# Kernel optimization log

Measured on AMD Instinct MI355X. Metric: run time of the kernel, lower is better.

## Reference

```python
import jax, jax.numpy as jnp
import numpy as np

B, S, E, H, P, F = 8, 512, 512, 8, 64, 2048
D = E // H  # head_dim = 64
EPS = 1e-5


def layernorm(x, g, b):
    mu = jnp.mean(x, axis=-1, keepdims=True)
    var = jnp.mean((x - mu) ** 2, axis=-1, keepdims=True)
    return (x - mu) * jax.lax.rsqrt(var + EPS) * g + b


def setup_inputs() -> dict:
    key = jax.random.key(0)
    ks = jax.random.split(key, 20)
    s = 1.0 / np.sqrt(E)
    inp = {
        "x": jax.random.normal(ks[0], (B, S, E), jnp.float32),
        "dist": jax.random.uniform(ks[1], (B, S, S), jnp.float32),
        "delatimes": jax.random.randint(ks[2], (B, S), 0, 128, jnp.int32),
        "mask": jnp.ones((B, S), jnp.int32),
        "wq_w": jax.random.uniform(ks[3], (E, E), jnp.float32, -s, s),
        "wq_b": jnp.zeros((E,), jnp.float32),
        "wk_w": jax.random.uniform(ks[4], (E, E), jnp.float32, -s, s),
        "wk_b": jnp.zeros((E,), jnp.float32),
        "wv_w": jax.random.uniform(ks[5], (E, E), jnp.float32, -s, s),
        "wv_b": jnp.zeros((E,), jnp.float32),
        "wo_w": jax.random.uniform(ks[6], (E, E), jnp.float32, -s, s),
        "wo_b": jnp.zeros((E,), jnp.float32),
        "pos_emb": jax.random.normal(ks[7], (2 * P + 1, D), jnp.float32),
        "w1": jax.random.uniform(ks[8], (E, F), jnp.float32, -s, s),
        "b1": jnp.zeros((F,), jnp.float32),
        "w2": jax.random.uniform(ks[9], (F, E), jnp.float32, -1.0 / np.sqrt(F), 1.0 / np.sqrt(F)),
        "b2": jnp.zeros((E,), jnp.float32),
        "ln1_g": jnp.ones((E,), jnp.float32),
        "ln1_b": jnp.zeros((E,), jnp.float32),
        "ln2_g": jnp.ones((E,), jnp.float32),
        "ln2_b": jnp.zeros((E,), jnp.float32),
    }
    return inp


def reference(x, dist, delatimes, mask, wq_w, wq_b, wk_w, wk_b, wv_w, wv_b,
              wo_w, wo_b, pos_emb, w1, b1, w2, b2, ln1_g, ln1_b, ln2_g, ln2_b):
    # relative-time embedding indices [B,S,S]
    rel = delatimes[:, None, :] - delatimes[:, :, None]
    idx = jnp.clip(rel, -P, P) + P
    z = pos_emb[idx]  # [B,S,S,D]

    def heads(t, w, b):
        return (t @ w + b).reshape(B, S, H, D).transpose(0, 2, 1, 3)  # [B,H,S,D]

    q = heads(x, wq_w, wq_b)
    k = heads(x, wk_w, wk_b)
    v = heads(x, wv_w, wv_b)

    scale = D ** -0.5
    scores = jnp.einsum('bhid,bhjd->bhij', q, k) + jnp.einsum('bhid,bijd->bhij', q, z)
    w = scores * scale + 0.6 * dist[:, None, :, :]
    pad = mask[:, None, None, :]  # [B,1,1,S]
    w = jnp.where(pad == 0, -1e9, w)
    aw = jax.nn.softmax(w, axis=-1)

    attn = jnp.einsum('bhij,bhjd->bhid', aw, v) + jnp.einsum('bhij,bijd->bhid', aw, z)
    concat = attn.transpose(0, 2, 1, 3).reshape(B, S, E)
    attn_out = layernorm(x + (concat @ wo_w + wo_b), ln1_g, ln1_b)

    ffn = jax.nn.relu(attn_out @ w1 + b1) @ w2 + b2
    return layernorm(attn_out + ffn, ln2_g, ln2_b)
```

## Files before the change

### kernel.cpp

```cpp
#include <hip/hip_runtime.h>
#include <hip/hip_bf16.h>

typedef __bf16 bf16x8 __attribute__((ext_vector_type(8)));
typedef float f32x4 __attribute__((ext_vector_type(4)));

#define TOKENS 4096
#define EDIM 512
#define FDIM 2048
#define SEQ 512
#define NHEAD 8
#define HDIM 64
#define QKVS 1536

__global__ __launch_bounds__(256) void prep(
    const float* __restrict__ wq_w, const float* __restrict__ wk_w,
    const float* __restrict__ wv_w, const float* __restrict__ wo_w,
    const float* __restrict__ w1, const float* __restrict__ w2,
    const float* __restrict__ x, const float* __restrict__ dist,
    const float* __restrict__ wq_b, const float* __restrict__ wk_b,
    const float* __restrict__ wv_b,
    __bf16* __restrict__ wqkvt, __bf16* __restrict__ wot,
    __bf16* __restrict__ w1t, __bf16* __restrict__ w2t,
    __bf16* __restrict__ xb, __bf16* __restrict__ distb,
    float* __restrict__ qkvb) {
  __shared__ float t[32][33];
  int bid = blockIdx.x;
  if (bid < 3072) {
    const float* src;
    __bf16* dst;
    int R = 512, C = 512, bx, by;
    if (bid < 1024) {
      int seg = bid >> 8, local = bid & 255;
      src = seg == 0 ? wq_w : seg == 1 ? wk_w : seg == 2 ? wv_w : wo_w;
      dst = seg == 0 ? wqkvt : seg == 1 ? wqkvt + 262144 : seg == 2 ? wqkvt + 524288 : wot;
      bx = local & 15; by = local >> 4;
    } else if (bid < 2048) {
      int local = bid - 1024; src = w1; dst = w1t; C = 2048;
      bx = local & 63; by = local >> 6;
    } else {
      int local = bid - 2048; src = w2; dst = w2t; R = 2048;
      bx = local & 15; by = local >> 4;
    }
    int c0 = bx * 32, r0 = by * 32;
    int tx = threadIdx.x & 31, ty = threadIdx.x >> 5;
    for (int rr = ty; rr < 32; rr += 8)
      t[rr][tx] = src[(size_t)(r0 + rr) * C + c0 + tx];
    __syncthreads();
    for (int rr = ty; rr < 32; rr += 8)
      dst[(size_t)(c0 + rr) * R + r0 + tx] = (__bf16)t[tx][rr];
  } else if (bid < 4096) {
    int i = (bid - 3072) * 256 + threadIdx.x;
    float4 a = ((const float4*)x)[i * 2];
    float4 b4 = ((const float4*)x)[i * 2 + 1];
    bf16x8 p;
    p[0] = (__bf16)a.x; p[1] = (__bf16)a.y; p[2] = (__bf16)a.z; p[3] = (__bf16)a.w;
    p[4] = (__bf16)b4.x; p[5] = (__bf16)b4.y; p[6] = (__bf16)b4.z; p[7] = (__bf16)b4.w;
    ((bf16x8*)xb)[i] = p;
  } else if (bid == 4096) {
    for (int i = threadIdx.x; i < 1536; i += 256)
      qkvb[i] = i < 512 ? wq_b[i] : i < 1024 ? wk_b[i - 512] : wv_b[i - 1024];
  } else {
    int i = (bid - 4097) * 256 + threadIdx.x;
    float4 a = ((const float4*)dist)[i * 2];
    float4 b4 = ((const float4*)dist)[i * 2 + 1];
    bf16x8 p;
    p[0] = (__bf16)a.x; p[1] = (__bf16)a.y; p[2] = (__bf16)a.z; p[3] = (__bf16)a.w;
    p[4] = (__bf16)b4.x; p[5] = (__bf16)b4.y; p[6] = (__bf16)b4.z; p[7] = (__bf16)b4.w;
    ((bf16x8*)distb)[i] = p;
  }
}

__device__ __forceinline__ void gl_lds16(const void* g, void* l) {
  __builtin_amdgcn_global_load_lds(
      (const __attribute__((address_space(1))) unsigned int*)(size_t)g,
      (__attribute__((address_space(3))) unsigned int*)(size_t)l, 16, 0, 0);
}

template <int BM, int BN>
__global__ __launch_bounds__(256) void gemm128(
    const __bf16* __restrict__ A, const __bf16* __restrict__ Bt,
    const float* __restrict__ bias, const float* __restrict__ resid,
    const __bf16* __restrict__ residb,
    float* __restrict__ Cf, __bf16* __restrict__ Cb,
    int M, int N, int K, int relu) {
  constexpr int MI = BM / 32, NI = BN / 32;
  __shared__ __attribute__((aligned(16))) __bf16 Asl[BM * 64];
  __shared__ __attribute__((aligned(16))) __bf16 Bsl[BN * 64];
  const int tid = threadIdx.x, w = tid >> 6, lane = tid & 63;
  const int c = lane & 15, g = lane >> 4;
  const int nwg = gridDim.x * gridDim.y;
  const int orig = blockIdx.y * gridDim.x + blockIdx.x;
  const int swz = (orig & 7) * (nwg >> 3) + (orig >> 3);
  const int m0 = (swz / gridDim.x) * BM, n0 = (swz % gridDim.x) * BN;
  const int wr = w >> 1, wc = w & 1;
  f32x4 acc[MI][NI] = {};
  const __bf16* Ab = A + (size_t)m0 * K;
  const __bf16* Bb = Bt + (size_t)n0 * K;

  for (int k0 = 0; k0 < K; k0 += 64) {
#pragma unroll
    for (int s = 0; s < BM / 32; s++) {
      int L = (s * 256 + tid) * 16;
      int row = L >> 7;
      int lslot = ((L >> 4) & 7) ^ (row & 7);
      gl_lds16(Ab + (size_t)row * K + k0 + lslot * 8,
               (char*)Asl + s * 4096 + w * 1024);
    }
#pragma unroll
    for (int s = 0; s < BN / 32; s++) {
      int L = (s * 256 + tid) * 16;
      int row = L >> 7;
      int lslot = ((L >> 4) & 7) ^ (row & 7);
      gl_lds16(Bb + (size_t)row * K + k0 + lslot * 8,
               (char*)Bsl + s * 4096 + w * 1024);
    }
    __syncthreads();

    bf16x8 af[MI][2], bfr[NI][2];
#pragma unroll
    for (int mi = 0; mi < MI; mi++)
#pragma unroll
      for (int ko = 0; ko < 2; ko++) {
        int row = wr * (BM / 2) + mi * 16 + c;
        int ps = (ko * 4 + g) ^ (row & 7);
        af[mi][ko] = *(const bf16x8*)&Asl[row * 64 + ps * 8];
      }
#pragma unroll
    for (int ni = 0; ni < NI; ni++)
#pragma unroll
      for (int ko = 0; ko < 2; ko++) {
        int row = wc * (BN / 2) + ni * 16 + c;
        int ps = (ko * 4 + g) ^ (row & 7);
        bfr[ni][ko] = *(const bf16x8*)&Bsl[row * 64 + ps * 8];
      }
#pragma unroll
    for (int mi = 0; mi < MI; mi++)
#pragma unroll
      for (int ni = 0; ni < NI; ni++) {
        acc[mi][ni] = __builtin_amdgcn_mfma_f32_16x16x32_bf16(af[mi][0], bfr[ni][0], acc[mi][ni], 0, 0, 0);
        acc[mi][ni] = __builtin_amdgcn_mfma_f32_16x16x32_bf16(af[mi][1], bfr[ni][1], acc[mi][ni], 0, 0, 0);
      }
    __syncthreads();
  }

#pragma unroll
  for (int mi = 0; mi < MI; mi++)
#pragma unroll
    for (int ni = 0; ni < NI; ni++)
#pragma unroll
      for (int r = 0; r < 4; r++) {
        int row = m0 + wr * (BM / 2) + mi * 16 + g * 4 + r;
        int col = n0 + wc * (BN / 2) + ni * 16 + c;
        float v = acc[mi][ni][r] + bias[col];
        if (resid) v += resid[(size_t)row * N + col];
        if (residb) v += (float)residb[(size_t)row * N + col];
        if (relu) v = fmaxf(v, 0.f);
        if (Cf) Cf[(size_t)row * N + col] = v;
        if (Cb) Cb[(size_t)row * N + col] = (__bf16)v;
      }
}

__device__ inline void cvt16(const float* __restrict__ src, __bf16* dst) {
  float4 f0 = *(const float4*)(src);
  float4 f1 = *(const float4*)(src + 4);
  float4 f2 = *(const float4*)(src + 8);
  float4 f3 = *(const float4*)(src + 12);
  bf16x8 p0, p1;
  p0[0]=(__bf16)f0.x; p0[1]=(__bf16)f0.y; p0[2]=(__bf16)f0.z; p0[3]=(__bf16)f0.w;
  p0[4]=(__bf16)f1.x; p0[5]=(__bf16)f1.y; p0[6]=(__bf16)f1.z; p0[7]=(__bf16)f1.w;
  p1[0]=(__bf16)f2.x; p1[1]=(__bf16)f2.y; p1[2]=(__bf16)f2.z; p1[3]=(__bf16)f2.w;
  p1[4]=(__bf16)f3.x; p1[5]=(__bf16)f3.y; p1[6]=(__bf16)f3.z; p1[7]=(__bf16)f3.w;
  *(bf16x8*)(dst) = p0;
  *(bf16x8*)(dst + 8) = p1;
}

__global__ __launch_bounds__(256) void qz_shift(
    const __bf16* __restrict__ qb, const float* __restrict__ pos_emb,
    const int* __restrict__ dtimes, __bf16* __restrict__ QZg) {
  __shared__ __attribute__((aligned(16))) __bf16 peL[144][72];
  __shared__ __attribute__((aligned(16))) __bf16 QL[64][72];
  __shared__ __attribute__((aligned(16))) float qzf[64][144];
  const int tid = threadIdx.x, w = tid >> 6, l = tid & 63, c = l & 15, g = l >> 4;
  const int bid = blockIdx.x, qt = bid & 7, bh = bid >> 3, h = bh & 7, b = bh >> 3;
  const int qbase = qt * 64;
  const int r = tid >> 2, d0 = (tid & 3) * 16;

  for (int s = 0; s < 3; s++) {
    int rr = r + s * 64;
    if (rr >= 144) break;
    if (rr < 129) {
      cvt16(pos_emb + rr * 64 + d0, &peL[rr][d0]);
    } else {
      bf16x8 z = {};
      *(bf16x8*)&peL[rr][d0] = z;
      *(bf16x8*)&peL[rr][d0 + 8] = z;
    }
  }
  {
    const __bf16* qp = qb + ((size_t)(b * SEQ + qbase + r)) * QKVS + h * HDIM + d0;
    *(bf16x8*)&QL[r][d0] = *(const bf16x8*)qp;
    *(bf16x8*)&QL[r][d0 + 8] = *(const bf16x8*)(qp + 8);
  }
  __syncthreads();

  bf16x8 aq0 = *(bf16x8*)&QL[w * 16 + c][g * 8];
  bf16x8 aq1 = *(bf16x8*)&QL[w * 16 + c][32 + g * 8];
  for (int n = 0; n < 9; n++) {
    f32x4 acc = {};
    bf16x8 b0 = *(bf16x8*)&peL[n * 16 + c][g * 8];
    bf16x8 b1 = *(bf16x8*)&peL[n * 16 + c][32 + g * 8];
    acc = __builtin_amdgcn_mfma_f32_16x16x32_bf16(aq0, b0, acc, 0, 0, 0);
    acc = __builtin_amdgcn_mfma_f32_16x16x32_bf16(aq1, b1, acc, 0, 0, 0);
    int t = n * 16 + c;
    for (int r4 = 0; r4 < 4; r4++) qzf[w * 16 + g * 4 + r4][t] = acc[r4];
  }
  __syncthreads();

  int dti = dtimes[b * SEQ + qbase + r];
  int t0 = (tid & 3) * 32;
  for (int q4 = 0; q4 < 4; q4++) {
    bf16x8 o;
    for (int e = 0; e < 8; e++) {
      int tau = t0 + q4 * 8 + e;
      int t = min(max(tau - dti, -64), 64) + 64;
      o[e] = (__bf16)qzf[r][t];
    }
    *(bf16x8*)(QZg + ((size_t)(bh * SEQ + qbase + r)) * 128 + t0 + q4 * 8) = o;
  }
}

#define KL_OFF 18432
__global__ __launch_bounds__(256) void attn_fused(
    const __bf16* __restrict__ qb, const __bf16* __restrict__ kb,
    const __bf16* __restrict__ vb, const __bf16* __restrict__ distb,
    const int* __restrict__ dtimes, const int* __restrict__ maskp,
    const __bf16* __restrict__ QZg, const float* __restrict__ pos_emb,
    __bf16* __restrict__ outb) {
  __shared__ __attribute__((aligned(16))) char smem[75776];
  auto QL  = (__bf16(*)[72])(smem);
  auto PL  = (__bf16(*)[72])(smem + 9216);
  char* KLb = smem + KL_OFF;
  auto VT  = (__bf16(*)[72])(smem + 26624);
  auto B1h = (__bf16(*)[72])(smem + 35840);
  auto qzL = (__bf16(*)[136])(smem + 54272);
  int* dtsL = (int*)(smem + 71680);
  int* mskL = (int*)(smem + 73728);
  auto CLs = (float(*)[136])(smem);
  auto peT = (__bf16(*)[136])(smem + 34816);

  const int tid = threadIdx.x, w = tid >> 6, l = tid & 63, c = l & 15, g = l >> 4;
  const int bid = blockIdx.x;
  const int qt = bid & 7, h = (bid >> 3) & 7, b = bid >> 6, bh = bid >> 3;
  const int qbase = qt * 64;
  const int r = tid >> 2, d0 = (tid & 3) * 16;
  const int vd = l, vj0 = w * 16;

  auto stageK = [&](int jt) {
#pragma unroll
    for (int s = 0; s < 2; s++) {
      int L = (s * 256 + tid) * 16;
      int row = L >> 7;
      int sl = ((L >> 4) & 7) ^ (row & 7);
      gl_lds16(kb + ((size_t)(b * SEQ + jt * 64 + row)) * QKVS + h * HDIM + sl * 8,
               KLb + s * 4096 + w * 1024);
    }
  };
  __bf16 vreg[16];
  float dA[16], dB[16];
  auto loadV = [&](int jt) {
    const __bf16* vp = vb + ((size_t)(b * SEQ + jt * 64 + vj0)) * QKVS + h * HDIM + vd;
#pragma unroll
    for (int q = 0; q < 16; q++) vreg[q] = vp[(size_t)q * QKVS];
  };
  auto loadD = [&](int jt, float (&dd)[16]) {
#pragma unroll
    for (int n = 0; n < 4; n++)
#pragma unroll
      for (int r4 = 0; r4 < 4; r4++) {
        int il = w * 16 + g * 4 + r4;
        dd[n * 4 + r4] =
            (float)distb[((size_t)(b * SEQ + qbase + il)) * SEQ + jt * 64 + n * 16 + c];
      }
  };

  stageK(0); loadV(0); loadD(0, dA);

  {
    const __bf16* qp = qb + ((size_t)(b * SEQ + qbase + r)) * QKVS + h * HDIM + d0;
    *(bf16x8*)&QL[r][d0] = *(const bf16x8*)qp;
    *(bf16x8*)&QL[r][d0 + 8] = *(const bf16x8*)(qp + 8);
  }
  {
    int ch = (tid & 3) * 32;
    const __bf16* src = QZg + ((size_t)(bh * SEQ + qbase + r)) * 128 + ch;
    for (int q4 = 0; q4 < 4; q4++)
      *(bf16x8*)&qzL[r][ch + q4 * 8] = *(const bf16x8*)(src + q4 * 8);
  }
  for (int idx = tid; idx < SEQ; idx += 256) {
    dtsL[idx] = dtimes[b * SEQ + idx];
    mskL[idx] = maskp[b * SEQ + idx];
  }
  {
    bf16x8 z = {};
    for (int idx = tid; idx < 128 * 9; idx += 256)
      *(bf16x8*)&B1h[idx / 9][(idx % 9) * 8] = z;
  }
  __syncthreads();

  bf16x8 aq0 = *(bf16x8*)&QL[w * 16 + c][g * 8];
  bf16x8 aq1 = *(bf16x8*)&QL[w * 16 + c][32 + g * 8];
  float lsum[4] = {0.f, 0.f, 0.f, 0.f};
  f32x4 Oacc[4] = {};
  f32x4 Cacc[8] = {};

  auto body = [&](int jt, float (&dcur)[16], float (&dnxt)[16]) {
    __syncthreads();
    {
      bf16x8 pv0, pv1;
#pragma unroll
      for (int q = 0; q < 8; q++) { pv0[q] = vreg[q]; pv1[q] = vreg[q + 8]; }
      *(bf16x8*)&VT[vd][vj0] = pv0;
      *(bf16x8*)&VT[vd][vj0 + 8] = pv1;
    }
    if (tid < 64) {
      if (jt > 0) {
        int tp = dtsL[(jt - 1) * 64 + tid], tn = dtsL[jt * 64 + tid];
        if (tp != tn) B1h[tp][tid] = (__bf16)0.f;
        B1h[tn][tid] = (__bf16)1.f;
      } else {
        B1h[dtsL[tid]][tid] = (__bf16)1.f;
      }
    }
    if (jt < 7) { loadV(jt + 1); loadD(jt + 1, dnxt); }
    __syncthreads();

#pragma unroll
    for (int n = 0; n < 4; n++) {
      f32x4 acc = {};
      int row = n * 16 + c;
      bf16x8 bk0 = *(const bf16x8*)(KLb + row * 128 + ((g ^ (row & 7)) * 16));
      bf16x8 bk1 = *(const bf16x8*)(KLb + row * 128 + (((g + 4) ^ (row & 7)) * 16));
      acc = __builtin_amdgcn_mfma_f32_16x16x32_bf16(aq0, bk0, acc, 0, 0, 0);
      acc = __builtin_amdgcn_mfma_f32_16x16x32_bf16(aq1, bk1, acc, 0, 0, 0);
      int jl = n * 16 + c, jg = jt * 64 + jl;
      int dtj = dtsL[jg];
      int mk = mskL[jg];
#pragma unroll
      for (int r4 = 0; r4 < 4; r4++) {
        int il = w * 16 + g * 4 + r4;
        float s = (acc[r4] + (float)qzL[il][dtj]) * 0.125f + 0.6f * dcur[n * 4 + r4];
        float p = mk ? __expf(s) : 0.f;
        lsum[r4] += p;
        PL[il][jl] = (__bf16)p;
      }
    }
    __syncthreads();
    if (jt < 7) stageK(jt + 1);

    bf16x8 ap0 = *(bf16x8*)&PL[w * 16 + c][g * 8];
    bf16x8 ap1 = *(bf16x8*)&PL[w * 16 + c][32 + g * 8];
#pragma unroll
    for (int dn = 0; dn < 4; dn++) {
      bf16x8 bv0 = *(bf16x8*)&VT[dn * 16 + c][g * 8];
      bf16x8 bv1 = *(bf16x8*)&VT[dn * 16 + c][32 + g * 8];
      Oacc[dn] = __builtin_amdgcn_mfma_f32_16x16x32_bf16(ap0, bv0, Oacc[dn], 0, 0, 0);
      Oacc[dn] = __builtin_amdgcn_mfma_f32_16x16x32_bf16(ap1, bv1, Oacc[dn], 0, 0, 0);
    }
#pragma unroll
    for (int tn = 0; tn < 8; tn++) {
      bf16x8 bz0 = *(bf16x8*)&B1h[tn * 16 + c][g * 8];
      bf16x8 bz1 = *(bf16x8*)&B1h[tn * 16 + c][32 + g * 8];
      Cacc[tn] = __builtin_amdgcn_mfma_f32_16x16x32_bf16(ap0, bz0, Cacc[tn], 0, 0, 0);
      Cacc[tn] = __builtin_amdgcn_mfma_f32_16x16x32_bf16(ap1, bz1, Cacc[tn], 0, 0, 0);
    }
  };
  for (int jt2 = 0; jt2 < 8; jt2 += 2) {
    body(jt2, dA, dB);
    body(jt2 + 1, dB, dA);
  }

  __syncthreads();
  {
    float4 z4 = {0.f, 0.f, 0.f, 0.f};
    for (int idx = tid; idx < 64 * 34; idx += 256) ((float4*)CLs)[idx] = z4;
  }
  for (int s = 0; s < 3; s++) {
    int t = r + s * 64;
    if (t < 129) {
      float vals[16];
      *(float4*)&vals[0]  = *(const float4*)(pos_emb + t * 64 + d0);
      *(float4*)&vals[4]  = *(const float4*)(pos_emb + t * 64 + d0 + 4);
      *(float4*)&vals[8]  = *(const float4*)(pos_emb + t * 64 + d0 + 8);
      *(float4*)&vals[12] = *(const float4*)(pos_emb + t * 64 + d0 + 12);
#pragma unroll
      for (int q = 0; q < 16; q++) peT[d0 + q][t] = (__bf16)vals[q];
    }
  }
  __syncthreads();

  {
    int dti_r4[4];
#pragma unroll
    for (int r4 = 0; r4 < 4; r4++) dti_r4[r4] = dtsL[qbase + w * 16 + g * 4 + r4];
#pragma unroll
    for (int tn = 0; tn < 8; tn++)
#pragma unroll
      for (int r4 = 0; r4 < 4; r4++) {
        int il = w * 16 + g * 4 + r4;
        int tau = tn * 16 + c, d = tau - dti_r4[r4];
        float val = Cacc[tn][r4];
        if (d <= -64) atomicAdd(&CLs[il][0], val);
        else if (d >= 64) atomicAdd(&CLs[il][128], val);
        else CLs[il][d + 64] = val;
      }
  }
  __syncthreads();

  float linv[4];
#pragma unroll
  for (int r4 = 0; r4 < 4; r4++) {
    float s = lsum[r4];
    for (int off = 1; off < 16; off <<= 1) s += __shfl_xor(s, off);
    linv[r4] = 1.0f / s;
  }

  f32x4 acc2[4] = {};
#pragma unroll
  for (int ks = 0; ks < 4; ks++) {
    const float* ap = &CLs[w * 16 + c][ks * 32 + g * 8];
    float4 a0 = *(const float4*)ap, a1 = *(const float4*)(ap + 4);
    bf16x8 af;
    af[0]=(__bf16)a0.x; af[1]=(__bf16)a0.y; af[2]=(__bf16)a0.z; af[3]=(__bf16)a0.w;
    af[4]=(__bf16)a1.x; af[5]=(__bf16)a1.y; af[6]=(__bf16)a1.z; af[7]=(__bf16)a1.w;
#pragma unroll
    for (int dn = 0; dn < 4; dn++) {
      bf16x8 bf = *(bf16x8*)&peT[dn * 16 + c][ks * 32 + g * 8];
      acc2[dn] = __builtin_amdgcn_mfma_f32_16x16x32_bf16(af, bf, acc2[dn], 0, 0, 0);
    }
  }
#pragma unroll
  for (int r4 = 0; r4 < 4; r4++) {
    int il = w * 16 + g * 4 + r4;
    float c128 = CLs[il][128];
#pragma unroll
    for (int dn = 0; dn < 4; dn++) {
      int d = dn * 16 + c;
      float y = acc2[dn][r4] + c128 * (float)peT[d][128];
      outb[((size_t)(b * SEQ + qbase + il)) * EDIM + h * HDIM + d] =
          (__bf16)((Oacc[dn][r4] + y) * linv[r4]);
    }
  }
}

__global__ __launch_bounds__(256) void ln_kernel(
    const float* __restrict__ in, const float* __restrict__ g,
    const float* __restrict__ bta, float* __restrict__ out,
    __bf16* __restrict__ outb) {
  int row = blockIdx.x * 4 + (threadIdx.x >> 6), lane = threadIdx.x & 63;
  const float* p = in + (size_t)row * EDIM;
  float4 v0 = *(const float4*)(p + lane * 8);
  float4 v1 = *(const float4*)(p + lane * 8 + 4);
  float vals[8] = {v0.x, v0.y, v0.z, v0.w, v1.x, v1.y, v1.z, v1.w};
  float s = 0.f;
  for (int j = 0; j < 8; j++) s += vals[j];
  for (int o = 32; o; o >>= 1) s += __shfl_xor(s, o);
  float mu = s * (1.0f / EDIM);
  float vs = 0.f;
  for (int j = 0; j < 8; j++) {
    vals[j] -= mu;
    vs += vals[j] * vals[j];
  }
  for (int o = 32; o; o >>= 1) vs += __shfl_xor(vs, o);
  float rs = rsqrtf(vs * (1.0f / EDIM) + 1e-5f);
  for (int j = 0; j < 8; j++) {
    int col = lane * 8 + j;
    float v = vals[j] * rs * g[col] + bta[col];
    if (out) out[(size_t)row * EDIM + col] = v;
    if (outb) outb[(size_t)row * EDIM + col] = (__bf16)v;
  }
}

extern "C" void kernel_launch(void* const* d_in, const int* in_sizes, int n_in,
                              void* d_out, int out_size, void* d_ws, size_t ws_size,
                              hipStream_t stream) {
  const float* x = (const float*)d_in[0];
  const float* dist = (const float*)d_in[1];
  const int* dtimes = (const int*)d_in[2];
  const int* maskp = (const int*)d_in[3];
  const float* wq_w = (const float*)d_in[4];
  const float* wq_b = (const float*)d_in[5];
  const float* wk_w = (const float*)d_in[6];
  const float* wk_b = (const float*)d_in[7];
  const float* wv_w = (const float*)d_in[8];
  const float* wv_b = (const float*)d_in[9];
  const float* wo_w = (const float*)d_in[10];
  const float* wo_b = (const float*)d_in[11];
  const float* pos_emb = (const float*)d_in[12];
  const float* w1 = (const float*)d_in[13];
  const float* b1 = (const float*)d_in[14];
  const float* w2 = (const float*)d_in[15];
  const float* b2 = (const float*)d_in[16];
  const float* ln1_g = (const float*)d_in[17];
  const float* ln1_b = (const float*)d_in[18];
  const float* ln2_g = (const float*)d_in[19];
  const float* ln2_b = (const float*)d_in[20];
  float* out = (float*)d_out;

  const int M = TOKENS;
  const size_t T = TOKENS;
  float* fws = (float*)d_ws;

  __bf16* qkvB   = (__bf16*)fws;
  float*  ln2in  = fws;
  float*  wo_out = fws + T * 768;
  __bf16* QZg    = (__bf16*)(fws + T * 1792);
  __bf16* attnob = (__bf16*)(fws + T * 2304);
  __bf16* hid    = (__bf16*)(fws + T * 2560);
  __bf16* attnb  = (__bf16*)(fws + T * 3584);
  __bf16* xb     = (__bf16*)(fws + T * 3840);
  __bf16* wqkvt  = (__bf16*)(fws + T * 4096);
  __bf16* wot    = wqkvt + 1536 * 512;
  __bf16* w1t    = wot + 512 * 512;
  __bf16* w2t    = w1t + 512 * 2048;
  __bf16* distb  = w2t + 2048 * 512;
  float*  qkvb   = (float*)(distb + 2097152);

  prep<<<5121, 256, 0, stream>>>(wq_w, wk_w, wv_w, wo_w, w1, w2, x, dist,
                                 wq_b, wk_b, wv_b,
                                 wqkvt, wot, w1t, w2t, xb, distb, qkvb);

  gemm128<64, 128><<<dim3(1536 / 128, M / 64), 256, 0, stream>>>(
      xb, wqkvt, qkvb, nullptr, nullptr, nullptr, qkvB, M, 1536, 512, 0);

  qz_shift<<<512, 256, 0, stream>>>(qkvB, pos_emb, dtimes, QZg);
  attn_fused<<<512, 256, 0, stream>>>(qkvB, qkvB + 512, qkvB + 1024, distb,
                                      dtimes, maskp, QZg, pos_emb, attnb);

  gemm128<64, 64><<<dim3(512 / 64, M / 64), 256, 0, stream>>>(
      attnb, wot, wo_b, x, nullptr, wo_out, nullptr, M, 512, 512, 0);
  ln_kernel<<<M / 4, 256, 0, stream>>>(wo_out, ln1_g, ln1_b, nullptr, attnob);

  gemm128<64, 128><<<dim3(2048 / 128, M / 64), 256, 0, stream>>>(
      attnob, w1t, b1, nullptr, nullptr, nullptr, hid, M, 2048, 512, 1);
  gemm128<64, 64><<<dim3(512 / 64, M / 64), 256, 0, stream>>>(
      hid, w2t, b2, nullptr, attnob, ln2in, nullptr, M, 512, 2048, 0);
  ln_kernel<<<M / 4, 256, 0, stream>>>(ln2in, ln2_g, ln2_b, out, nullptr);
}
```

Before: 249.7 us.

## Fuse QZ shift kernel into attention prologue and use exp2 with prescaled constants

Removes the separate qz_shift launch: the attention kernel now computes q·pos_emb with MFMA into shared memory, gathers the clipped shifted relative-time row into registers, and writes it to its qzL buffer directly. This avoids a kernel launch and the global write and read of the QZ intermediate. The block index mapping is reordered so batch varies fastest. Softmax exponent now uses exp2f with log2e folded into the scale constants. The prologue gets longer and shared memory regions are aliased, which may lengthen per-block startup.

After: 245.6 us. Within noise of the previous version (-1.6%).

```diff
diff --git a/kernel.cpp b/kernel.cpp
--- a/kernel.cpp
+++ b/kernel.cpp
@@ -174,17 +174,68 @@
   *(bf16x8*)(dst + 8) = p1;
 }
 
-__global__ __launch_bounds__(256) void qz_shift(
-    const __bf16* __restrict__ qb, const float* __restrict__ pos_emb,
-    const int* __restrict__ dtimes, __bf16* __restrict__ QZg) {
-  __shared__ __attribute__((aligned(16))) __bf16 peL[144][72];
-  __shared__ __attribute__((aligned(16))) __bf16 QL[64][72];
-  __shared__ __attribute__((aligned(16))) float qzf[64][144];
+#define KL_OFF 18432
+__global__ __launch_bounds__(256) void attn_fused(
+    const __bf16* __restrict__ qb, const __bf16* __restrict__ kb,
+    const __bf16* __restrict__ vb, const __bf16* __restrict__ distb,
+    const int* __restrict__ dtimes, const int* __restrict__ maskp,
+    const float* __restrict__ pos_emb, __bf16* __restrict__ outb) {
+  __shared__ __attribute__((aligned(16))) char smem[75776];
+  auto QL  = (__bf16(*)[72])(smem);
+  auto PL  = (__bf16(*)[72])(smem + 9216);
+  char* KLb = smem + KL_OFF;
+  auto VT  = (__bf16(*)[72])(smem + 26624);
+  auto B1h = (__bf16(*)[72])(smem + 35840);
+  auto qzL = (__bf16(*)[136])(smem + 54272);
+  int* dtsL = (int*)(smem + 71680);
+  int* mskL = (int*)(smem + 73728);
+  auto peL = (__bf16(*)[72])(smem + 9216);
+  auto qzf = (__bf16(*)[144])(smem + 29952);
+  auto CLs = (float(*)[136])(smem);
+  auto peT = (__bf16(*)[136])(smem + 34816);
+
   const int tid = threadIdx.x, w = tid >> 6, l = tid & 63, c = l & 15, g = l >> 4;
-  const int bid = blockIdx.x, qt = bid & 7, bh = bid >> 3, h = bh & 7, b = bh >> 3;
+  const int bid = blockIdx.x;
+  const int b = bid & 7, h = (bid >> 3) & 7, qt = bid >> 6;
   const int qbase = qt * 64;
   const int r = tid >> 2, d0 = (tid & 3) * 16;
-
+  const int vd = l, vj0 = w * 16;
+
+  auto stageK = [&](int jt) {
+#pragma unroll
+    for (int s = 0; s < 2; s++) {
+      int L = (s * 256 + tid) * 16;
+      int row = L >> 7;
+      int sl = ((L >> 4) & 7) ^ (row & 7);
+      gl_lds16(kb + ((size_t)(b * SEQ + jt * 64 + row)) * QKVS + h * HDIM + sl * 8,
+               KLb + s * 4096 + w * 1024);
+    }
+  };
+  __bf16 vreg[16];
+  float dA[16], dB[16];
+  auto loadV = [&](int jt) {
+    const __bf16* vp = vb + ((size_t)(b * SEQ + jt * 64 + vj0)) * QKVS + h * HDIM + vd;
+#pragma unroll
+    for (int q = 0; q < 16; q++) vreg[q] = vp[(size_t)q * QKVS];
+  };
+  auto loadD = [&](int jt, float (&dd)[16]) {
+#pragma unroll
+    for (int n = 0; n < 4; n++)
+#pragma unroll
+      for (int r4 = 0; r4 < 4; r4++) {
+        int il = w * 16 + g * 4 + r4;
+        dd[n * 4 + r4] =
+            (float)distb[((size_t)(b * SEQ + qbase + il)) * SEQ + jt * 64 + n * 16 + c];
+      }
+  };
+
+  loadV(0); loadD(0, dA);
+
+  {
+    const __bf16* qp = qb + ((size_t)(b * SEQ + qbase + r)) * QKVS + h * HDIM + d0;
+    *(bf16x8*)&QL[r][d0] = *(const bf16x8*)qp;
+    *(bf16x8*)&QL[r][d0 + 8] = *(const bf16x8*)(qp + 8);
+  }
   for (int s = 0; s < 3; s++) {
     int rr = r + s * 64;
     if (rr >= 144) break;
@@ -196,15 +247,15 @@
       *(bf16x8*)&peL[rr][d0 + 8] = z;
     }
   }
-  {
-    const __bf16* qp = qb + ((size_t)(b * SEQ + qbase + r)) * QKVS + h * HDIM + d0;
-    *(bf16x8*)&QL[r][d0] = *(const bf16x8*)qp;
-    *(bf16x8*)&QL[r][d0 + 8] = *(const bf16x8*)(qp + 8);
+  for (int idx = tid; idx < SEQ; idx += 256) {
+    dtsL[idx] = dtimes[b * SEQ + idx];
+    mskL[idx] = maskp[b * SEQ + idx];
   }
   __syncthreads();
 
   bf16x8 aq0 = *(bf16x8*)&QL[w * 16 + c][g * 8];
   bf16x8 aq1 = *(bf16x8*)&QL[w * 16 + c][32 + g * 8];
+#pragma unroll
   for (int n = 0; n < 9; n++) {
     f32x4 acc = {};
     bf16x8 b0 = *(bf16x8*)&peL[n * 16 + c][g * 8];
@@ -212,106 +263,46 @@
     acc = __builtin_amdgcn_mfma_f32_16x16x32_bf16(aq0, b0, acc, 0, 0, 0);
     acc = __builtin_amdgcn_mfma_f32_16x16x32_bf16(aq1, b1, acc, 0, 0, 0);
     int t = n * 16 + c;
-    for (int r4 = 0; r4 < 4; r4++) qzf[w * 16 + g * 4 + r4][t] = acc[r4];
-  }
-  __syncthreads();
-
-  int dti = dtimes[b * SEQ + qbase + r];
-  int t0 = (tid & 3) * 32;
-  for (int q4 = 0; q4 < 4; q4++) {
-    bf16x8 o;
-    for (int e = 0; e < 8; e++) {
-      int tau = t0 + q4 * 8 + e;
-      int t = min(max(tau - dti, -64), 64) + 64;
-      o[e] = (__bf16)qzf[r][t];
-    }
-    *(bf16x8*)(QZg + ((size_t)(bh * SEQ + qbase + r)) * 128 + t0 + q4 * 8) = o;
-  }
-}
-
-#define KL_OFF 18432
-__global__ __launch_bounds__(256) void attn_fused(
-    const __bf16* __restrict__ qb, const __bf16* __restrict__ kb,
-    const __bf16* __restrict__ vb, const __bf16* __restrict__ distb,
-    const int* __restrict__ dtimes, const int* __restrict__ maskp,
-    const __bf16* __restrict__ QZg, const float* __restrict__ pos_emb,
-    __bf16* __restrict__ outb) {
-  __shared__ __attribute__((aligned(16))) char smem[75776];
-  auto QL  = (__bf16(*)[72])(smem);
-  auto PL  = (__bf16(*)[72])(smem + 9216);
-  char* KLb = smem + KL_OFF;
-  auto VT  = (__bf16(*)[72])(smem + 26624);
-  auto B1h = (__bf16(*)[72])(smem + 35840);
-  auto qzL = (__bf16(*)[136])(smem + 54272);
-  int* dtsL = (int*)(smem + 71680);
-  int* mskL = (int*)(smem + 73728);
-  auto CLs = (float(*)[136])(smem);
-  auto peT = (__bf16(*)[136])(smem + 34816);
-
-  const int tid = threadIdx.x, w = tid >> 6, l = tid & 63, c = l & 15, g = l >> 4;
-  const int bid = blockIdx.x;
-  const int qt = bid & 7, h = (bid >> 3) & 7, b = bid >> 6, bh = bid >> 3;
-  const int qbase = qt * 64;
-  const int r = tid >> 2, d0 = (tid & 3) * 16;
-  const int vd = l, vj0 = w * 16;
-
-  auto stageK = [&](int jt) {
-#pragma unroll
-    for (int s = 0; s < 2; s++) {
-      int L = (s * 256 + tid) * 16;
-      int row = L >> 7;
-      int sl = ((L >> 4) & 7) ^ (row & 7);
-      gl_lds16(kb + ((size_t)(b * SEQ + jt * 64 + row)) * QKVS + h * HDIM + sl * 8,
-               KLb + s * 4096 + w * 1024);
-    }
-  };
-  __bf16 vreg[16];
-  float dA[16], dB[16];
-  auto loadV = [&](int jt) {
-    const __bf16* vp = vb + ((size_t)(b * SEQ + jt * 64 + vj0)) * QKVS + h * HDIM + vd;
-#pragma unroll
-    for (int q = 0; q < 16; q++) vreg[q] = vp[(size_t)q * QKVS];
-  };
-  auto loadD = [&](int jt, float (&dd)[16]) {
-#pragma unroll
-    for (int n = 0; n < 4; n++)
-#pragma unroll
-      for (int r4 = 0; r4 < 4; r4++) {
-        int il = w * 16 + g * 4 + r4;
-        dd[n * 4 + r4] =
-            (float)distb[((size_t)(b * SEQ + qbase + il)) * SEQ + jt * 64 + n * 16 + c];
-      }
-  };
-
-  stageK(0); loadV(0); loadD(0, dA);
-
+#pragma unroll
+    for (int r4 = 0; r4 < 4; r4++) qzf[w * 16 + g * 4 + r4][t] = (__bf16)acc[r4];
+  }
+  __syncthreads();
+
+  __bf16 qzv[32];
   {
-    const __bf16* qp = qb + ((size_t)(b * SEQ + qbase + r)) * QKVS + h * HDIM + d0;
-    *(bf16x8*)&QL[r][d0] = *(const bf16x8*)qp;
-    *(bf16x8*)&QL[r][d0 + 8] = *(const bf16x8*)(qp + 8);
-  }
+    int dti = dtsL[qbase + r];
+    int t0 = (tid & 3) * 32;
+#pragma unroll
+    for (int e = 0; e < 32; e++) {
+      int tt = min(max(t0 + e - dti, -64), 64) + 64;
+      qzv[e] = qzf[r][tt];
+    }
+  }
+  __syncthreads();
+
   {
-    int ch = (tid & 3) * 32;
-    const __bf16* src = QZg + ((size_t)(bh * SEQ + qbase + r)) * 128 + ch;
-    for (int q4 = 0; q4 < 4; q4++)
-      *(bf16x8*)&qzL[r][ch + q4 * 8] = *(const bf16x8*)(src + q4 * 8);
-  }
-  for (int idx = tid; idx < SEQ; idx += 256) {
-    dtsL[idx] = dtimes[b * SEQ + idx];
-    mskL[idx] = maskp[b * SEQ + idx];
+    int t0 = (tid & 3) * 32;
+#pragma unroll
+    for (int q4 = 0; q4 < 4; q4++) {
+      bf16x8 o;
+#pragma unroll
+      for (int e = 0; e < 8; e++) o[e] = qzv[q4 * 8 + e];
+      *(bf16x8*)&qzL[r][t0 + q4 * 8] = o;
+    }
   }
   {
     bf16x8 z = {};
     for (int idx = tid; idx < 128 * 9; idx += 256)
       *(bf16x8*)&B1h[idx / 9][(idx % 9) * 8] = z;
   }
-  __syncthreads();
-
-  bf16x8 aq0 = *(bf16x8*)&QL[w * 16 + c][g * 8];
-  bf16x8 aq1 = *(bf16x8*)&QL[w * 16 + c][32 + g * 8];
+  stageK(0);
+  __syncthreads();
+
   float lsum[4] = {0.f, 0.f, 0.f, 0.f};
   f32x4 Oacc[4] = {};
   f32x4 Cacc[8] = {};
+  const float SCL = 0.125f * 1.44269504f;
+  const float DCO = 0.6f * 1.44269504f;
 
   auto body = [&](int jt, float (&dcur)[16], float (&dnxt)[16]) {
     __syncthreads();
@@ -348,8 +339,8 @@
 #pragma unroll
       for (int r4 = 0; r4 < 4; r4++) {
         int il = w * 16 + g * 4 + r4;
-        float s = (acc[r4] + (float)qzL[il][dtj]) * 0.125f + 0.6f * dcur[n * 4 + r4];
-        float p = mk ? __expf(s) : 0.f;
+        float s = (acc[r4] + (float)qzL[il][dtj]) * SCL + DCO * dcur[n * 4 + r4];
+        float p = mk ? exp2f(s) : 0.f;
         lsum[r4] += p;
         PL[il][jl] = (__bf16)p;
       }
@@ -513,7 +504,6 @@
   __bf16* qkvB   = (__bf16*)fws;
   float*  ln2in  = fws;
   float*  wo_out = fws + T * 768;
-  __bf16* QZg    = (__bf16*)(fws + T * 1792);
   __bf16* attnob = (__bf16*)(fws + T * 2304);
   __bf16* hid    = (__bf16*)(fws + T * 2560);
   __bf16* attnb  = (__bf16*)(fws + T * 3584);
@@ -532,9 +522,8 @@
   gemm128<64, 128><<<dim3(1536 / 128, M / 64), 256, 0, stream>>>(
       xb, wqkvt, qkvb, nullptr, nullptr, nullptr, qkvB, M, 1536, 512, 0);
 
-  qz_shift<<<512, 256, 0, stream>>>(qkvB, pos_emb, dtimes, QZg);
   attn_fused<<<512, 256, 0, stream>>>(qkvB, qkvB + 512, qkvB + 1024, distb,
-                                      dtimes, maskp, QZg, pos_emb, attnb);
+                                      dtimes, maskp, pos_emb, attnb);
 
   gemm128<64, 64><<<dim3(512 / 64, M / 64), 256, 0, stream>>>(
       attnb, wot, wo_b, x, nullptr, wo_out, nullptr, M, 512, 512, 0);
```
